# Optimization experiments

Measured on AMD Instinct MI355X. Metric: run time of the kernel, lower is better.

Reference implementation:

```python
import jax, jax.numpy as jnp
import numpy as np

B, C_IN, C_OUT, MODES, LENGTH = 32, 32, 32, 64, 16384


def dht(x):
    # Discrete Hartley Transform via complex FFT: H = Re(X) - Im(X) = sum x * cas
    X = jnp.fft.fft(x, axis=-1)
    return X.real - X.imag


def flip_periodic(x):
    # Z[0] = x[0], Z[k] = x[N-k] for k >= 1
    return jnp.concatenate([x[..., :1], x[..., 1:][..., ::-1]], axis=-1)


def setup_inputs() -> dict:
    key = jax.random.key(0)
    k1, k2, k3 = jax.random.split(key, 3)
    x = jax.random.normal(k1, (B, C_IN, LENGTH), dtype=jnp.float32)
    scale = 1.0 / (C_IN * C_OUT)
    weights1 = scale * jax.random.uniform(k2, (C_IN, C_OUT, MODES), dtype=jnp.float32)
    phase_weights = jax.random.uniform(k3, (C_IN, C_OUT, MODES), dtype=jnp.float32)
    return {"x": x, "weights1": weights1, "phase_weights": phase_weights}


def reference(x, weights1, phase_weights):
    batch, length = x.shape[0], x.shape[-1]
    m = weights1.shape[-1]
    out_ch = weights1.shape[1]

    x_ht = dht(x)                      # [b, in, L]
    xm = x_ht[:, :, :m]                # truncated spectrum [b, in, m]

    # Hartley convolution theorem: even/odd decomposition of the kernel
    y_flip = flip_periodic(weights1)
    y_even = 0.5 * (weights1 + y_flip)
    y_odd = 0.5 * (weights1 - y_flip)
    z = (jnp.einsum('bix,iox->box', xm, y_even)
         + jnp.einsum('bix,iox->box', flip_periodic(xm), y_odd))  # [b, out, m]

    # phase multiply (per-(out, mode); see notes on original in-place broadcast)
    z = z * jnp.sin(phase_weights)[0]  # [out, m] broadcast over batch

    out_ht = jnp.zeros((batch, out_ch, length), dtype=x.dtype).at[:, :, :m].set(z)
    # inverse DHT: DHT is involutory up to 1/n
    return dht(out_ht) / length
```

## Files before the change

### kernel.cpp

```cpp
#include <hip/hip_runtime.h>
#include <math.h>

#define N_LEN 16384
#define NMODES 64
#define NROWS 1024
#define PAD 72
#define REV_SCALE 6.103515625e-05f

typedef __bf16  bf16x8  __attribute__((ext_vector_type(8)));
typedef float   floatx16 __attribute__((ext_vector_type(16)));

__device__ inline unsigned short f2b(float f) {
    unsigned u = __float_as_uint(f);
    u += 0x7fffu + ((u >> 16) & 1u);
    return (unsigned short)(u >> 16);
}

__device__ inline unsigned short cas_bf16(unsigned k) {
    float rev = (float)k * REV_SCALE;
#if __has_builtin(__builtin_amdgcn_sinf) && __has_builtin(__builtin_amdgcn_cosf)
    float s = __builtin_amdgcn_sinf(rev);
    float c = __builtin_amdgcn_cosf(rev);
#else
    float s, c;
    sincosf(rev * 6.28318530717958647692f, &s, &c);
#endif
    return f2b(c + s);
}

#define G1_RB 128

__global__ __launch_bounds__(256) void gemm1(const float* __restrict__ x,
                                             float* __restrict__ part,
                                             int ntiles) {
    __shared__ unsigned short xs[G1_RB * PAD];
    __shared__ unsigned short ts[64 * PAD];
    const int tid  = threadIdx.x;
    const int lane = tid & 63;
    const int w    = tid >> 6;
    const int q    = lane >> 5;
    const int m    = lane & 31;
    const int row0 = blockIdx.x * G1_RB;
    const int n0   = blockIdx.y * (ntiles * 64);

    const int mrow = tid >> 2;
    const int nl0  = (tid & 3) * 16;

    floatx16 acc0, acc1;
#pragma unroll
    for (int i = 0; i < 16; ++i) { acc0[i] = 0.f; acc1[i] = 0.f; }

    float4 xr[8];
    {
        const int base = n0;
#pragma unroll
        for (int it = 0; it < 8; ++it) {
            int cid = it * 256 + tid, rr = cid >> 4, cc = (cid & 15) * 4;
            xr[it] = *(const float4*)(x + (size_t)(row0 + rr) * N_LEN + base + cc);
        }
    }

    for (int t = 0; t < ntiles; ++t) {
        __syncthreads();
#pragma unroll
        for (int it = 0; it < 8; ++it) {
            int cid = it * 256 + tid, rr = cid >> 4, cc = (cid & 15) * 4;
            ushort4 v;
            v.x = f2b(xr[it].x); v.y = f2b(xr[it].y);
            v.z = f2b(xr[it].z); v.w = f2b(xr[it].w);
            *(ushort4*)(xs + rr * PAD + cc) = v;
        }
        if (t + 1 < ntiles) {
            const int base = n0 + (t + 1) * 64;
#pragma unroll
            for (int it = 0; it < 8; ++it) {
                int cid = it * 256 + tid, rr = cid >> 4, cc = (cid & 15) * 4;
                xr[it] = *(const float4*)(x + (size_t)(row0 + rr) * N_LEN + base + cc);
            }
        }
        {
            unsigned nb = (unsigned)(n0 + t * 64 + nl0);
            unsigned k  = ((unsigned)mrow * nb) & (N_LEN - 1);
            unsigned pk[8];
#pragma unroll
            for (int j = 0; j < 8; ++j) {
                unsigned lo = cas_bf16(k); k = (k + mrow) & (N_LEN - 1);
                unsigned hi = cas_bf16(k); k = (k + mrow) & (N_LEN - 1);
                pk[j] = lo | (hi << 16);
            }
            uint4* dst = (uint4*)(ts + mrow * PAD + nl0);
            dst[0] = make_uint4(pk[0], pk[1], pk[2], pk[3]);
            dst[1] = make_uint4(pk[4], pk[5], pk[6], pk[7]);
        }
        __syncthreads();
#pragma unroll
        for (int ks = 0; ks < 4; ++ks) {
            bf16x8 a  = *(const bf16x8*)(xs + (w * 32 + m) * PAD + ks * 16 + q * 8);
            bf16x8 b0 = *(const bf16x8*)(ts + (m)          * PAD + ks * 16 + q * 8);
            bf16x8 b1 = *(const bf16x8*)(ts + (32 + m)     * PAD + ks * 16 + q * 8);
            acc0 = __builtin_amdgcn_mfma_f32_32x32x16_bf16(a, b0, acc0, 0, 0, 0);
            acc1 = __builtin_amdgcn_mfma_f32_32x32x16_bf16(a, b1, acc1, 0, 0, 0);
        }
    }

    float* pb = part + ((size_t)blockIdx.y * NROWS + row0 + w * 32) * NMODES;
#pragma unroll
    for (int r = 0; r < 16; ++r) {
        int rowt = (r & 3) + 8 * (r >> 2) + 4 * q;
        pb[rowt * NMODES + m]      = acc0[r];
        pb[rowt * NMODES + 32 + m] = acc1[r];
    }
}

__global__ __launch_bounds__(256) void reduce_xm(const float* __restrict__ part,
                                                 float* __restrict__ xm, int S) {
    int gid = blockIdx.x * 256 + threadIdx.x;
    const float* p = part + gid;
    float a0 = 0.f, a1 = 0.f, a2 = 0.f, a3 = 0.f;
#pragma unroll 4
    for (int s = 0; s < S; s += 4) {
        a0 += p[(size_t)(s + 0) * (NROWS * NMODES)];
        a1 += p[(size_t)(s + 1) * (NROWS * NMODES)];
        a2 += p[(size_t)(s + 2) * (NROWS * NMODES)];
        a3 += p[(size_t)(s + 3) * (NROWS * NMODES)];
    }
    xm[gid] = (a0 + a1) + (a2 + a3);
}

__global__ __launch_bounds__(256) void mixk(const float* __restrict__ xm,
                                            const float* __restrict__ w1,
                                            const float* __restrict__ pw,
                                            unsigned short* __restrict__ zb) {
    int k = threadIdx.x & 63;
    int wave = threadIdx.x >> 6;
    int b = blockIdx.x;
    int o = blockIdx.y * 4 + wave;
    int kf = (NMODES - k) & 63;

    float acc = 0.f;
#pragma unroll 4
    for (int i = 0; i < 32; ++i) {
        float xv  = xm[(size_t)(b * 32 + i) * NMODES + k];
        float xvf = xm[(size_t)(b * 32 + i) * NMODES + kf];
        float w   = w1[(size_t)(i * 32 + o) * NMODES + k];
        float wf  = w1[(size_t)(i * 32 + o) * NMODES + kf];
        acc = fmaf(xv, 0.5f * (w + wf), acc);
        acc = fmaf(xvf, 0.5f * (w - wf), acc);
    }
    const float sc = 1.0f / (float)N_LEN;
    zb[(size_t)(b * 32 + o) * NMODES + k] =
        f2b(acc * sinf(pw[(size_t)o * NMODES + k]) * sc);
}

#define G2_NB 256

__global__ __launch_bounds__(256) void gemm2(const unsigned short* __restrict__ zb,
                                             float* __restrict__ out) {
    __shared__ unsigned short tts[G2_NB * PAD];
    __shared__ unsigned short zs[64 * PAD];
    const int tid  = threadIdx.x;
    const int lane = tid & 63;
    const int w    = tid >> 6;
    const int q    = lane >> 5;
    const int m    = lane & 31;
    const int wr   = w & 1;
    const int wn   = w >> 1;
    const int row0 = blockIdx.x * 64;
    const int nb0  = blockIdx.y * G2_NB;

    uint4 zr[2];
#pragma unroll
    for (int it = 0; it < 2; ++it) {
        int idx = it * 256 + tid, rr = idx >> 3, c = idx & 7;
        zr[it] = *(const uint4*)(zb + (size_t)(row0 + rr) * NMODES + c * 8);
    }

    {
        unsigned n = (unsigned)(nb0 + tid);
        unsigned k = 0;
        uint4* dst = (uint4*)(tts + tid * PAD);
#pragma unroll
        for (int g = 0; g < 8; ++g) {
            unsigned pk[4];
#pragma unroll
            for (int j = 0; j < 4; ++j) {
                unsigned lo = cas_bf16(k); k = (k + n) & (N_LEN - 1);
                unsigned hi = cas_bf16(k); k = (k + n) & (N_LEN - 1);
                pk[j] = lo | (hi << 16);
            }
            dst[g] = make_uint4(pk[0], pk[1], pk[2], pk[3]);
        }
    }

#pragma unroll
    for (int it = 0; it < 2; ++it) {
        int idx = it * 256 + tid, rr = idx >> 3, c = idx & 7;
        *(uint4*)(zs + rr * PAD + c * 8) = zr[it];
    }
    __syncthreads();

    floatx16 acc[4];
#pragma unroll
    for (int nt = 0; nt < 4; ++nt)
#pragma unroll
        for (int i = 0; i < 16; ++i) acc[nt][i] = 0.f;

#pragma unroll
    for (int ks = 0; ks < 4; ++ks) {
        bf16x8 a = *(const bf16x8*)(zs + (wr * 32 + m) * PAD + ks * 16 + q * 8);
#pragma unroll
        for (int nt = 0; nt < 4; ++nt) {
            bf16x8 b = *(const bf16x8*)(tts + (wn * 128 + nt * 32 + m) * PAD + ks * 16 + q * 8);
            acc[nt] = __builtin_amdgcn_mfma_f32_32x32x16_bf16(a, b, acc[nt], 0, 0, 0);
        }
    }

#pragma unroll
    for (int nt = 0; nt < 4; ++nt) {
#pragma unroll
        for (int r = 0; r < 16; ++r) {
            int rowt = (r & 3) + 8 * (r >> 2) + 4 * q;
            out[(size_t)(row0 + wr * 32 + rowt) * N_LEN + nb0 + wn * 128 + nt * 32 + m]
                = acc[nt][r];
        }
    }
}

extern "C" void kernel_launch(void* const* d_in, const int* in_sizes, int n_in,
                              void* d_out, int out_size, void* d_ws, size_t ws_size,
                              hipStream_t stream) {
    const float* x  = (const float*)d_in[0];
    const float* w1 = (const float*)d_in[1];
    const float* pw = (const float*)d_in[2];
    float* out = (float*)d_out;

    int S = 64;
    while (S > 8) {
        size_t need = (size_t)S * NROWS * NMODES * 4u
                    + (size_t)NROWS * NMODES * 4u
                    + (size_t)NROWS * NMODES * 2u;
        if (need <= ws_size) break;
        S >>= 1;
    }
    const int ntiles = N_LEN / S / 64;

    char* p = (char*)d_ws;
    float*          P   = (float*)p;                    p += (size_t)S * NROWS * NMODES * 4;
    float*          XM  = (float*)p;                    p += (size_t)NROWS * NMODES * 4;
    unsigned short* ZB  = (unsigned short*)p;

    gemm1<<<dim3(NROWS / G1_RB, S), dim3(256), 0, stream>>>(x, P, ntiles);

    reduce_xm<<<dim3(NROWS * NMODES / 256), dim3(256), 0, stream>>>(P, XM, S);

    mixk<<<dim3(32, 8), dim3(256), 0, stream>>>(XM, w1, pw, ZB);

    gemm2<<<dim3(NROWS / 64, N_LEN / G2_NB), dim3(256), 0, stream>>>(ZB, out);
}
```

Measured before the change: 134.1 us.

## Replace split-K partial buffer and reduce kernel with atomic accumulation in gemm1

The forward DHT GEMM no longer writes per-split partial sums to a large workspace that a separate reduce kernel then sums. Each block now atomically adds its 32x32 tile into a zeroed xm buffer. The row block size is halved to 64 and the split is fixed at 64, giving 16x64 blocks of four waves each. This drops one kernel launch and the partial-buffer write and read traffic, in exchange for a memset, float atomic contention and nondeterministic summation order.

After: 137.0 us. +2.2%, slower.

```diff
diff --git a/kernel.cpp b/kernel.cpp
--- a/kernel.cpp
+++ b/kernel.cpp
@@ -6,6 +6,7 @@
 #define NROWS 1024
 #define PAD 72
 #define REV_SCALE 6.103515625e-05f
+#define SPLIT 64
 
 typedef __bf16  bf16x8  __attribute__((ext_vector_type(8)));
 typedef float   floatx16 __attribute__((ext_vector_type(16)));
@@ -28,10 +29,10 @@
     return f2b(c + s);
 }
 
-#define G1_RB 128
+#define G1_RB 64
 
 __global__ __launch_bounds__(256) void gemm1(const float* __restrict__ x,
-                                             float* __restrict__ part,
+                                             float* __restrict__ xm,
                                              int ntiles) {
     __shared__ unsigned short xs[G1_RB * PAD];
     __shared__ unsigned short ts[64 * PAD];
@@ -40,21 +41,23 @@
     const int w    = tid >> 6;
     const int q    = lane >> 5;
     const int m    = lane & 31;
+    const int wr   = w & 1;
+    const int wm   = w >> 1;
     const int row0 = blockIdx.x * G1_RB;
     const int n0   = blockIdx.y * (ntiles * 64);
 
     const int mrow = tid >> 2;
     const int nl0  = (tid & 3) * 16;
 
-    floatx16 acc0, acc1;
-#pragma unroll
-    for (int i = 0; i < 16; ++i) { acc0[i] = 0.f; acc1[i] = 0.f; }
-
-    float4 xr[8];
+    floatx16 acc;
+#pragma unroll
+    for (int i = 0; i < 16; ++i) acc[i] = 0.f;
+
+    float4 xr[4];
     {
         const int base = n0;
 #pragma unroll
-        for (int it = 0; it < 8; ++it) {
+        for (int it = 0; it < 4; ++it) {
             int cid = it * 256 + tid, rr = cid >> 4, cc = (cid & 15) * 4;
             xr[it] = *(const float4*)(x + (size_t)(row0 + rr) * N_LEN + base + cc);
         }
@@ -63,7 +66,7 @@
     for (int t = 0; t < ntiles; ++t) {
         __syncthreads();
 #pragma unroll
-        for (int it = 0; it < 8; ++it) {
+        for (int it = 0; it < 4; ++it) {
             int cid = it * 256 + tid, rr = cid >> 4, cc = (cid & 15) * 4;
             ushort4 v;
             v.x = f2b(xr[it].x); v.y = f2b(xr[it].y);
@@ -73,7 +76,7 @@
         if (t + 1 < ntiles) {
             const int base = n0 + (t + 1) * 64;
 #pragma unroll
-            for (int it = 0; it < 8; ++it) {
+            for (int it = 0; it < 4; ++it) {
                 int cid = it * 256 + tid, rr = cid >> 4, cc = (cid & 15) * 4;
                 xr[it] = *(const float4*)(x + (size_t)(row0 + rr) * N_LEN + base + cc);
             }
@@ -95,36 +98,18 @@
         __syncthreads();
 #pragma unroll
         for (int ks = 0; ks < 4; ++ks) {
-            bf16x8 a  = *(const bf16x8*)(xs + (w * 32 + m) * PAD + ks * 16 + q * 8);
-            bf16x8 b0 = *(const bf16x8*)(ts + (m)          * PAD + ks * 16 + q * 8);
-            bf16x8 b1 = *(const bf16x8*)(ts + (32 + m)     * PAD + ks * 16 + q * 8);
-            acc0 = __builtin_amdgcn_mfma_f32_32x32x16_bf16(a, b0, acc0, 0, 0, 0);
-            acc1 = __builtin_amdgcn_mfma_f32_32x32x16_bf16(a, b1, acc1, 0, 0, 0);
-        }
-    }
-
-    float* pb = part + ((size_t)blockIdx.y * NROWS + row0 + w * 32) * NMODES;
+            bf16x8 a = *(const bf16x8*)(xs + (wr * 32 + m) * PAD + ks * 16 + q * 8);
+            bf16x8 b = *(const bf16x8*)(ts + (wm * 32 + m) * PAD + ks * 16 + q * 8);
+            acc = __builtin_amdgcn_mfma_f32_32x32x16_bf16(a, b, acc, 0, 0, 0);
+        }
+    }
+
+    float* pb = xm + (size_t)(row0 + wr * 32) * NMODES + wm * 32;
 #pragma unroll
     for (int r = 0; r < 16; ++r) {
         int rowt = (r & 3) + 8 * (r >> 2) + 4 * q;
-        pb[rowt * NMODES + m]      = acc0[r];
-        pb[rowt * NMODES + 32 + m] = acc1[r];
-    }
-}
-
-__global__ __launch_bounds__(256) void reduce_xm(const float* __restrict__ part,
-                                                 float* __restrict__ xm, int S) {
-    int gid = blockIdx.x * 256 + threadIdx.x;
-    const float* p = part + gid;
-    float a0 = 0.f, a1 = 0.f, a2 = 0.f, a3 = 0.f;
-#pragma unroll 4
-    for (int s = 0; s < S; s += 4) {
-        a0 += p[(size_t)(s + 0) * (NROWS * NMODES)];
-        a1 += p[(size_t)(s + 1) * (NROWS * NMODES)];
-        a2 += p[(size_t)(s + 2) * (NROWS * NMODES)];
-        a3 += p[(size_t)(s + 3) * (NROWS * NMODES)];
-    }
-    xm[gid] = (a0 + a1) + (a2 + a3);
+        atomicAdd(pb + rowt * NMODES + m, acc[r]);
+    }
 }
 
 __global__ __launch_bounds__(256) void mixk(const float* __restrict__ xm,
@@ -234,24 +219,15 @@
     const float* pw = (const float*)d_in[2];
     float* out = (float*)d_out;
 
-    int S = 64;
-    while (S > 8) {
-        size_t need = (size_t)S * NROWS * NMODES * 4u
-                    + (size_t)NROWS * NMODES * 4u
-                    + (size_t)NROWS * NMODES * 2u;
-        if (need <= ws_size) break;
-        S >>= 1;
-    }
-    const int ntiles = N_LEN / S / 64;
+    const int ntiles = N_LEN / SPLIT / 64;
 
     char* p = (char*)d_ws;
-    float*          P   = (float*)p;                    p += (size_t)S * NROWS * NMODES * 4;
-    float*          XM  = (float*)p;                    p += (size_t)NROWS * NMODES * 4;
+    float*          XM  = (float*)p;           p += (size_t)NROWS * NMODES * 4;
     unsigned short* ZB  = (unsigned short*)p;
 
-    gemm1<<<dim3(NROWS / G1_RB, S), dim3(256), 0, stream>>>(x, P, ntiles);
-
-    reduce_xm<<<dim3(NROWS * NMODES / 256), dim3(256), 0, stream>>>(P, XM, S);
+    hipMemsetAsync(XM, 0, (size_t)NROWS * NMODES * 4, stream);
+
+    gemm1<<<dim3(NROWS / G1_RB, SPLIT), dim3(256), 0, stream>>>(x, XM, ntiles);
 
     mixk<<<dim3(32, 8), dim3(256), 0, stream>>>(XM, w1, pw, ZB);
 
```
